# Optimization experiments

Measured on AMD Instinct MI355X. Metric: run time of the kernel, lower is better.

The kernel has to match this reference:

```python
import jax, jax.numpy as jnp
import numpy as np

H = 1024
BATCH, T = 16, 2048

def setup_inputs() -> dict:
    key = jax.random.key(0)
    k1, k2, k3, k4 = jax.random.split(key, 4)
    scale = 1.0 / (H ** 0.5)
    return {
        "u_sequence": jax.random.normal(k1, (BATCH, T, 1), dtype=jnp.float32),
        "A": jax.random.normal(k2, (H, H), dtype=jnp.float32) * scale,
        "B": jax.random.normal(k3, (H, 1), dtype=jnp.float32) * scale,
        "C": jax.random.normal(k4, (1, H), dtype=jnp.float32) * scale,
        "D": jnp.zeros((1,), dtype=jnp.float32),
    }

def reference(u_sequence, A, B, C, D):
    # u_sequence: [Bt, T, 1]
    u = u_sequence[..., 0]            # [Bt, T]
    b_vec = B[:, 0]                   # [H]

    def step(h, u_t):
        # h: [Bt, H], u_t: [Bt]
        h_new = h @ A.T + u_t[:, None] * b_vec[None, :]
        return h_new, h_new

    h0 = jnp.zeros((u.shape[0], H), dtype=u.dtype)
    _, h_stack = jax.lax.scan(step, h0, u.T)   # h_stack: [T, Bt, H]
    h_stack = jnp.swapaxes(h_stack, 0, 1)      # [Bt, T, H]
    y = jnp.einsum("bth,h->bt", h_stack, C[0]) + u * D[0]
    return y[..., None]                         # [Bt, T, 1]
```

## Files before the change

kernel.cpp:

```cpp
#include <hip/hip_runtime.h>

#define HDIM 1024
#define TLEN 2048
#define NBATCH 16

typedef short bf16x8 __attribute__((ext_vector_type(8)));
typedef float floatx4 __attribute__((ext_vector_type(4)));
typedef unsigned short ushort_t;

__device__ __forceinline__ ushort_t f2bf(float x) {
  unsigned u = __float_as_uint(x);
  unsigned r = (u + 0x7FFFu + ((u >> 16) & 1u)) >> 16;
  return (ushort_t)r;
}
__device__ __forceinline__ float bf2f(ushort_t h) {
  return __uint_as_float(((unsigned)h) << 16);
}

#define LSTR 40
#define TSTR 71

__global__ __launch_bounds__(256) void prep(const float* __restrict__ A,
    const float* __restrict__ Bv, const float* __restrict__ Cv,
    ushort_t* __restrict__ Ah, ushort_t* __restrict__ Am, ushort_t* __restrict__ Al,
    ushort_t* __restrict__ ATh, ushort_t* __restrict__ ATm, ushort_t* __restrict__ ATl,
    float* __restrict__ Vc, float* __restrict__ U) {
  __shared__ ushort_t Lt[3 * 64 * TSTR];
  const int tid = threadIdx.x;
  if (blockIdx.x >= 256) {
    int i = (blockIdx.x - 256) * 256 + tid;
    if (i < HDIM) Vc[i] = Bv[i];
    else U[i - HDIM] = Cv[i - HDIM];
    return;
  }
  const int row0 = (blockIdx.x >> 4) * 64, col0 = (blockIdx.x & 15) * 64;
  const int r = tid >> 2, q = tid & 3;
  ushort_t hs[16], ms[16], ls[16];
#pragma unroll
  for (int c4 = 0; c4 < 4; ++c4) {
    float4 a = *(const float4*)&A[(row0 + r) * HDIM + col0 + q * 16 + c4 * 4];
    float av[4] = {a.x, a.y, a.z, a.w};
#pragma unroll
    for (int i = 0; i < 4; ++i) {
      float z = av[i];
      ushort_t h = f2bf(z); float r1 = z - bf2f(h);
      ushort_t mq = f2bf(r1); float r2 = r1 - bf2f(mq);
      ushort_t lq = f2bf(r2);
      hs[c4 * 4 + i] = h; ms[c4 * 4 + i] = mq; ls[c4 * 4 + i] = lq;
    }
  }
  size_t go = (size_t)(row0 + r) * HDIM + col0 + q * 16;
  *(uint4*)&Ah[go] = ((uint4*)hs)[0]; *(uint4*)&Ah[go + 8] = ((uint4*)hs)[1];
  *(uint4*)&Am[go] = ((uint4*)ms)[0]; *(uint4*)&Am[go + 8] = ((uint4*)ms)[1];
  *(uint4*)&Al[go] = ((uint4*)ls)[0]; *(uint4*)&Al[go + 8] = ((uint4*)ls)[1];
#pragma unroll
  for (int i = 0; i < 16; ++i) {
    int c = q * 16 + i;
    Lt[0 * 64 * TSTR + r * TSTR + c] = hs[i];
    Lt[1 * 64 * TSTR + r * TSTR + c] = ms[i];
    Lt[2 * 64 * TSTR + r * TSTR + c] = ls[i];
  }
  __syncthreads();
  const int c = tid >> 2, q2 = tid & 3;
  ushort_t* dsts[3] = {ATh, ATm, ATl};
#pragma unroll
  for (int s = 0; s < 3; ++s) {
    ushort_t tmp[16];
#pragma unroll
    for (int rr = 0; rr < 16; ++rr) tmp[rr] = Lt[s * 64 * TSTR + (q2 * 16 + rr) * TSTR + c];
    size_t gt = (size_t)(col0 + c) * HDIM + row0 + q2 * 16;
    *(uint4*)&dsts[s][gt] = ((uint4*)tmp)[0];
    *(uint4*)&dsts[s][gt + 8] = ((uint4*)tmp)[1];
  }
}

template <int MODE, int NC, bool SIX, bool WRITEL>
__global__ __launch_bounds__(256) void sq_mfma(
    const ushort_t* __restrict__ Xh, const ushort_t* __restrict__ Xm,
    const ushort_t* __restrict__ Xl,
    const ushort_t* __restrict__ XTh, const ushort_t* __restrict__ XTm,
    const ushort_t* __restrict__ XTl,
    ushort_t* __restrict__ Zh, ushort_t* __restrict__ Zm, ushort_t* __restrict__ Zl,
    ushort_t* __restrict__ ZTh, ushort_t* __restrict__ ZTm, ushort_t* __restrict__ ZTl,
    const float* __restrict__ Af, const float* __restrict__ Bvf,
    float* __restrict__ VU) {
  __shared__ ushort_t sm[6 * 64 * LSTR];
  const int tid = threadIdx.x;

  if (blockIdx.x >= 256) {
    const int tb = blockIdx.x - 256;
    const int wv = tb * 4 + (tid >> 6);
    const int lane = tid & 63;
    if (MODE == 0) {
      float acc = 0.f;
      for (int k = lane; k < HDIM; k += 64) acc += Af[(size_t)wv * HDIM + k] * Bvf[k];
      for (int off = 32; off; off >>= 1) acc += __shfl_down(acc, off);
      if (lane == 0) VU[HDIM + wv] = acc;
    } else {
      const ushort_t* Ph = (MODE == 1) ? Xh : XTh;
      const ushort_t* Pm = (MODE == 1) ? Xm : XTm;
      float acc[NC];
#pragma unroll
      for (int n = 0; n < NC; ++n) acc[n] = 0.f;
      for (int k = lane; k < HDIM; k += 64) {
        float a = bf2f(Ph[(size_t)wv * HDIM + k]) + bf2f(Pm[(size_t)wv * HDIM + k]);
#pragma unroll
        for (int n = 0; n < NC; ++n) acc[n] += a * VU[(size_t)n * HDIM + k];
      }
#pragma unroll
      for (int n = 0; n < NC; ++n) {
        float s = acc[n];
        for (int off = 32; off; off >>= 1) s += __shfl_down(s, off);
        if (lane == 0) VU[(size_t)(NC + n) * HDIM + wv] = s;
      }
    }
    return;
  }

  const int bb = blockIdx.x;
  const int xcd = bb & 7, slot = bb >> 3;
  const int tr = 4 * (xcd >> 1) + (slot >> 3);
  const int tc = 8 * (xcd & 1) + (slot & 7);
  const int row0 = tr * 64, col0 = tc * 64;

  const int AH = 0, AM = 64 * LSTR, AL = 2 * 64 * LSTR;
  const int BH = 3 * 64 * LSTR, BM = 4 * 64 * LSTR, BL = 5 * 64 * LSTR;
  const int w = tid >> 6, l = tid & 63, li = l & 15, quad = l >> 4;
  const int sr = tid >> 2, sq4 = tid & 3;

  floatx4 acc0 = {0.f, 0.f, 0.f, 0.f}, acc1 = acc0, acc2 = acc0, acc3 = acc0;

  const int aoff = (w * 16 + li) * LSTR + quad * 8;
  const int b0o = (0 * 16 + li) * LSTR + quad * 8;
  const int b1o = (1 * 16 + li) * LSTR + quad * 8;
  const int b2o = (2 * 16 + li) * LSTR + quad * 8;
  const int b3o = (3 * 16 + li) * LSTR + quad * 8;
  const int soff = sr * LSTR + sq4 * 8;
  const size_t gA = (size_t)(row0 + sr) * HDIM + sq4 * 8;
  const size_t gB = (size_t)(col0 + sr) * HDIM + sq4 * 8;

  uint4 pa0 = *(const uint4*)&Xh[gA], pa1 = *(const uint4*)&Xm[gA];
  uint4 pb0 = *(const uint4*)&XTh[gB], pb1 = *(const uint4*)&XTm[gB];
  uint4 pa2, pb2;
  if (SIX) { pa2 = *(const uint4*)&Xl[gA]; pb2 = *(const uint4*)&XTl[gB]; }

  for (int k0 = 0; k0 < HDIM; k0 += 32) {
    __syncthreads();
    *(uint4*)&sm[AH + soff] = pa0;
    *(uint4*)&sm[AM + soff] = pa1;
    *(uint4*)&sm[BH + soff] = pb0;
    *(uint4*)&sm[BM + soff] = pb1;
    if (SIX) {
      *(uint4*)&sm[AL + soff] = pa2;
      *(uint4*)&sm[BL + soff] = pb2;
    }
    __syncthreads();
    if (k0 + 32 < HDIM) {
      pa0 = *(const uint4*)&Xh[gA + k0 + 32];
      pa1 = *(const uint4*)&Xm[gA + k0 + 32];
      pb0 = *(const uint4*)&XTh[gB + k0 + 32];
      pb1 = *(const uint4*)&XTm[gB + k0 + 32];
      if (SIX) {
        pa2 = *(const uint4*)&Xl[gA + k0 + 32];
        pb2 = *(const uint4*)&XTl[gB + k0 + 32];
      }
    }
    bf16x8 ah = *(const bf16x8*)&sm[AH + aoff];
    bf16x8 am = *(const bf16x8*)&sm[AM + aoff];
    bf16x8 al;
    if (SIX) al = *(const bf16x8*)&sm[AL + aoff];
    {
      bf16x8 bh = *(const bf16x8*)&sm[BH + b0o];
      bf16x8 bm = *(const bf16x8*)&sm[BM + b0o];
      acc0 = __builtin_amdgcn_mfma_f32_16x16x32_bf16(ah, bh, acc0, 0, 0, 0);
      acc0 = __builtin_amdgcn_mfma_f32_16x16x32_bf16(ah, bm, acc0, 0, 0, 0);
      acc0 = __builtin_amdgcn_mfma_f32_16x16x32_bf16(am, bh, acc0, 0, 0, 0);
      acc0 = __builtin_amdgcn_mfma_f32_16x16x32_bf16(am, bm, acc0, 0, 0, 0);
      if (SIX) {
        bf16x8 bl = *(const bf16x8*)&sm[BL + b0o];
        acc0 = __builtin_amdgcn_mfma_f32_16x16x32_bf16(ah, bl, acc0, 0, 0, 0);
        acc0 = __builtin_amdgcn_mfma_f32_16x16x32_bf16(al, bh, acc0, 0, 0, 0);
      }
    }
    {
      bf16x8 bh = *(const bf16x8*)&sm[BH + b1o];
      bf16x8 bm = *(const bf16x8*)&sm[BM + b1o];
      acc1 = __builtin_amdgcn_mfma_f32_16x16x32_bf16(ah, bh, acc1, 0, 0, 0);
      acc1 = __builtin_amdgcn_mfma_f32_16x16x32_bf16(ah, bm, acc1, 0, 0, 0);
      acc1 = __builtin_amdgcn_mfma_f32_16x16x32_bf16(am, bh, acc1, 0, 0, 0);
      acc1 = __builtin_amdgcn_mfma_f32_16x16x32_bf16(am, bm, acc1, 0, 0, 0);
      if (SIX) {
        bf16x8 bl = *(const bf16x8*)&sm[BL + b1o];
        acc1 = __builtin_amdgcn_mfma_f32_16x16x32_bf16(ah, bl, acc1, 0, 0, 0);
        acc1 = __builtin_amdgcn_mfma_f32_16x16x32_bf16(al, bh, acc1, 0, 0, 0);
      }
    }
    {
      bf16x8 bh = *(const bf16x8*)&sm[BH + b2o];
      bf16x8 bm = *(const bf16x8*)&sm[BM + b2o];
      acc2 = __builtin_amdgcn_mfma_f32_16x16x32_bf16(ah, bh, acc2, 0, 0, 0);
      acc2 = __builtin_amdgcn_mfma_f32_16x16x32_bf16(ah, bm, acc2, 0, 0, 0);
      acc2 = __builtin_amdgcn_mfma_f32_16x16x32_bf16(am, bh, acc2, 0, 0, 0);
      acc2 = __builtin_amdgcn_mfma_f32_16x16x32_bf16(am, bm, acc2, 0, 0, 0);
      if (SIX) {
        bf16x8 bl = *(const bf16x8*)&sm[BL + b2o];
        acc2 = __builtin_amdgcn_mfma_f32_16x16x32_bf16(ah, bl, acc2, 0, 0, 0);
        acc2 = __builtin_amdgcn_mfma_f32_16x16x32_bf16(al, bh, acc2, 0, 0, 0);
      }
    }
    {
      bf16x8 bh = *(const bf16x8*)&sm[BH + b3o];
      bf16x8 bm = *(const bf16x8*)&sm[BM + b3o];
      acc3 = __builtin_amdgcn_mfma_f32_16x16x32_bf16(ah, bh, acc3, 0, 0, 0);
      acc3 = __builtin_amdgcn_mfma_f32_16x16x32_bf16(ah, bm, acc3, 0, 0, 0);
      acc3 = __builtin_amdgcn_mfma_f32_16x16x32_bf16(am, bh, acc3, 0, 0, 0);
      acc3 = __builtin_amdgcn_mfma_f32_16x16x32_bf16(am, bm, acc3, 0, 0, 0);
      if (SIX) {
        bf16x8 bl = *(const bf16x8*)&sm[BL + b3o];
        acc3 = __builtin_amdgcn_mfma_f32_16x16x32_bf16(ah, bl, acc3, 0, 0, 0);
        acc3 = __builtin_amdgcn_mfma_f32_16x16x32_bf16(al, bh, acc3, 0, 0, 0);
      }
    }
  }

  __syncthreads();
  floatx4 accs[4] = {acc0, acc1, acc2, acc3};
#pragma unroll
  for (int j = 0; j < 4; ++j) {
#pragma unroll
    for (int e = 0; e < 4; ++e) {
      float z = accs[j][e];
      int rl = w * 16 + quad * 4 + e;
      int cl = j * 16 + li;
      size_t go = (size_t)(row0 + rl) * HDIM + col0 + cl;
      ushort_t h = f2bf(z); float r1 = z - bf2f(h);
      ushort_t mq = f2bf(r1);
      Zh[go] = h; Zm[go] = mq;
      sm[0 * 64 * TSTR + rl * TSTR + cl] = h;
      sm[1 * 64 * TSTR + rl * TSTR + cl] = mq;
      if (WRITEL) {
        ushort_t lq = f2bf(r1 - bf2f(mq));
        Zl[go] = lq;
        sm[2 * 64 * TSTR + rl * TSTR + cl] = lq;
      }
    }
  }
  __syncthreads();
  const int c = tid >> 2, q2 = tid & 3;
  ushort_t* dsts[3] = {ZTh, ZTm, ZTl};
  const int npass = WRITEL ? 3 : 2;
#pragma unroll
  for (int s = 0; s < 3; ++s) {
    if (s >= npass) break;
    ushort_t tmp[16];
#pragma unroll
    for (int rr = 0; rr < 16; ++rr) tmp[rr] = sm[s * 64 * TSTR + (q2 * 16 + rr) * TSTR + c];
    size_t gt = (size_t)(col0 + c) * HDIM + row0 + q2 * 16;
    *(uint4*)&dsts[s][gt] = ((uint4*)tmp)[0];
    *(uint4*)&dsts[s][gt + 8] = ((uint4*)tmp)[1];
  }
}

__global__ __launch_bounds__(256) void utail8(const ushort_t* __restrict__ PTh,
                                              const ushort_t* __restrict__ PTm,
                                              float* __restrict__ U, int dstbase) {
  const int wv = blockIdx.x * 4 + (threadIdx.x >> 6);
  const int lane = threadIdx.x & 63;
  float acc[8];
#pragma unroll
  for (int m = 0; m < 8; ++m) acc[m] = 0.f;
  const float* Usrc = U + (size_t)(dstbase - 8) * HDIM;
  for (int k = lane; k < HDIM; k += 64) {
    float a = bf2f(PTh[(size_t)wv * HDIM + k]) + bf2f(PTm[(size_t)wv * HDIM + k]);
#pragma unroll
    for (int m = 0; m < 8; ++m) acc[m] += a * Usrc[(size_t)m * HDIM + k];
  }
#pragma unroll
  for (int m = 0; m < 8; ++m) {
    float s = acc[m];
    for (int off = 32; off; off >>= 1) s += __shfl_down(s, off);
    if (lane == 0) U[(size_t)(dstbase + m) * HDIM + wv] = s;
  }
}

__global__ __launch_bounds__(256) void wavedotK(const float* __restrict__ U,
                                                const float* __restrict__ Vc,
                                                float* __restrict__ Km) {
  int wv = (blockIdx.x * blockDim.x + threadIdx.x) >> 6;
  int lane = threadIdx.x & 63;
  if (wv >= 32 * 64) return;
  int mr = wv >> 6;
  int nc = wv & 63;
  float s = 0.f;
  for (int k = lane; k < HDIM; k += 64) s += U[mr * HDIM + k] * Vc[nc * HDIM + k];
  for (int off = 32; off; off >>= 1) s += __shfl_down(s, off);
  if (lane == 0) Km[wv] = s;
}

__global__ __launch_bounds__(256) void convk2(const float* __restrict__ u,
                                              const float* __restrict__ Km,
                                              const float* __restrict__ Dv,
                                              float* __restrict__ y) {
  __shared__ float ks[256];
  __shared__ float us[512];
  const int tt = threadIdx.x;
  const int t0 = blockIdx.x * 256;
  const int b = blockIdx.y;
  const float* ub = u + (size_t)b * TLEN;
  const int t = t0 + tt;
  float s = Dv[0] * ub[t];
  for (int mc = 0; mc <= t0; mc += 256) {
    __syncthreads();
    ks[tt] = Km[mc + tt];
    int w0 = t0 - mc - 255;
    int g0 = w0 + tt;
    us[tt] = (g0 >= 0) ? ub[g0] : 0.f;
    int g1 = w0 + 256 + tt;
    us[256 + tt] = (g1 < TLEN) ? ub[g1] : 0.f;
    __syncthreads();
    if (mc < t0) {
#pragma unroll 4
      for (int r = 0; r < 256; r += 4) {
        float4 kv = *(const float4*)&ks[r];
        s += kv.x * us[tt - r + 255];
        s += kv.y * us[tt - r + 254];
        s += kv.z * us[tt - r + 253];
        s += kv.w * us[tt - r + 252];
      }
    } else {
      for (int r = 0; r <= tt; ++r) s += ks[r] * us[tt - r + 255];
    }
  }
  y[(size_t)b * TLEN + t] = s;
}

extern "C" void kernel_launch(void* const* d_in, const int* in_sizes, int n_in,
                              void* d_out, int out_size, void* d_ws, size_t ws_size,
                              hipStream_t stream) {
  const float* u  = (const float*)d_in[0];
  const float* A  = (const float*)d_in[1];
  const float* Bv = (const float*)d_in[2];
  const float* Cv = (const float*)d_in[3];
  const float* Dv = (const float*)d_in[4];
  float* out = (float*)d_out;

  char* wsb = (char*)d_ws;
  size_t off = 0;
  ushort_t* S[2][6];
  for (int s = 0; s < 2; ++s)
    for (int a = 0; a < 6; ++a) { S[s][a] = (ushort_t*)(wsb + off); off += (size_t)2 << 20; }
  float* Vc = (float*)(wsb + off); off += 64 * HDIM * 4;
  float* U  = (float*)(wsb + off); off += 32 * HDIM * 4;
  float* Km = (float*)(wsb + off); off += TLEN * 4;

  const dim3 gsq(512);

#define SQ(MODE, NC, SIX, WRL, IN, OUT, VU)                                    \
  sq_mfma<MODE, NC, SIX, WRL><<<gsq, 256, 0, stream>>>(                        \
      S[IN][0], S[IN][1], S[IN][2], S[IN][3], S[IN][4], S[IN][5],              \
      S[OUT][0], S[OUT][1], S[OUT][2], S[OUT][3], S[OUT][4], S[OUT][5],        \
      A, Bv, VU)

  prep<<<dim3(264), 256, 0, stream>>>(A, Bv, Cv,
      S[0][0], S[0][1], S[0][2], S[0][3], S[0][4], S[0][5], Vc, U);

  SQ(0, 1,  true,  true,  0, 1, Vc);
  SQ(1, 2,  true,  true,  1, 0, Vc);
  SQ(1, 4,  true,  true,  0, 1, Vc);
  SQ(1, 8,  true,  false, 1, 0, Vc);
  SQ(1, 16, false, false, 0, 1, Vc);
  SQ(1, 32, false, false, 1, 0, Vc);
  SQ(2, 1,  false, false, 0, 1, U);
  SQ(2, 2,  false, false, 1, 0, U);
  SQ(2, 4,  false, false, 0, 1, U);
#undef SQ

  utail8<<<dim3(256), 256, 0, stream>>>(S[1][3], S[1][4], U, 8);
  utail8<<<dim3(256), 256, 0, stream>>>(S[1][3], S[1][4], U, 16);
  utail8<<<dim3(256), 256, 0, stream>>>(S[1][3], S[1][4], U, 24);

  wavedotK<<<dim3(512), 256, 0, stream>>>(U, Vc, Km);
  convk2<<<dim3(TLEN / 256, NBATCH), 256, 0, stream>>>(u, Km, Dv, out);
}
```

Baseline: 333.4 us.

## Load MFMA operands directly from global memory with register double-buffering

Replaces the LDS-staged main loop of the split-bf16 squaring GEMM with operand fragments read straight from global memory into registers, using a two-stage ping-pong over 32-wide K chunks. This drops the two barriers per K step and the LDS store/load traffic, and shrinks shared memory to what the epilogue transpose needs. In exchange, each wave redundantly fetches the B fragments for all four column tiles (more global/L2 traffic, since there is no intra-block sharing), and register pressure rises from holding two full sets of operands.

Measured after the change: 576.1 us. 1.73x slower.

```diff
diff --git a/kernel.cpp b/kernel.cpp
--- a/kernel.cpp
+++ b/kernel.cpp
@@ -17,7 +17,6 @@
   return __uint_as_float(((unsigned)h) << 16);
 }
 
-#define LSTR 40
 #define TSTR 71
 
 __global__ __launch_bounds__(256) void prep(const float* __restrict__ A,
@@ -84,7 +83,7 @@
     ushort_t* __restrict__ ZTh, ushort_t* __restrict__ ZTm, ushort_t* __restrict__ ZTl,
     const float* __restrict__ Af, const float* __restrict__ Bvf,
     float* __restrict__ VU) {
-  __shared__ ushort_t sm[6 * 64 * LSTR];
+  __shared__ ushort_t sm[3 * 64 * TSTR];
   const int tid = threadIdx.x;
 
   if (blockIdx.x >= 256) {
@@ -123,108 +122,60 @@
   const int tc = 8 * (xcd & 1) + (slot & 7);
   const int row0 = tr * 64, col0 = tc * 64;
 
-  const int AH = 0, AM = 64 * LSTR, AL = 2 * 64 * LSTR;
-  const int BH = 3 * 64 * LSTR, BM = 4 * 64 * LSTR, BL = 5 * 64 * LSTR;
   const int w = tid >> 6, l = tid & 63, li = l & 15, quad = l >> 4;
-  const int sr = tid >> 2, sq4 = tid & 3;
-
-  floatx4 acc0 = {0.f, 0.f, 0.f, 0.f}, acc1 = acc0, acc2 = acc0, acc3 = acc0;
-
-  const int aoff = (w * 16 + li) * LSTR + quad * 8;
-  const int b0o = (0 * 16 + li) * LSTR + quad * 8;
-  const int b1o = (1 * 16 + li) * LSTR + quad * 8;
-  const int b2o = (2 * 16 + li) * LSTR + quad * 8;
-  const int b3o = (3 * 16 + li) * LSTR + quad * 8;
-  const int soff = sr * LSTR + sq4 * 8;
-  const size_t gA = (size_t)(row0 + sr) * HDIM + sq4 * 8;
-  const size_t gB = (size_t)(col0 + sr) * HDIM + sq4 * 8;
-
-  uint4 pa0 = *(const uint4*)&Xh[gA], pa1 = *(const uint4*)&Xm[gA];
-  uint4 pb0 = *(const uint4*)&XTh[gB], pb1 = *(const uint4*)&XTm[gB];
-  uint4 pa2, pb2;
-  if (SIX) { pa2 = *(const uint4*)&Xl[gA]; pb2 = *(const uint4*)&XTl[gB]; }
-
-  for (int k0 = 0; k0 < HDIM; k0 += 32) {
-    __syncthreads();
-    *(uint4*)&sm[AH + soff] = pa0;
-    *(uint4*)&sm[AM + soff] = pa1;
-    *(uint4*)&sm[BH + soff] = pb0;
-    *(uint4*)&sm[BM + soff] = pb1;
-    if (SIX) {
-      *(uint4*)&sm[AL + soff] = pa2;
-      *(uint4*)&sm[BL + soff] = pb2;
-    }
-    __syncthreads();
-    if (k0 + 32 < HDIM) {
-      pa0 = *(const uint4*)&Xh[gA + k0 + 32];
-      pa1 = *(const uint4*)&Xm[gA + k0 + 32];
-      pb0 = *(const uint4*)&XTh[gB + k0 + 32];
-      pb1 = *(const uint4*)&XTm[gB + k0 + 32];
-      if (SIX) {
-        pa2 = *(const uint4*)&Xl[gA + k0 + 32];
-        pb2 = *(const uint4*)&XTl[gB + k0 + 32];
-      }
-    }
-    bf16x8 ah = *(const bf16x8*)&sm[AH + aoff];
-    bf16x8 am = *(const bf16x8*)&sm[AM + aoff];
-    bf16x8 al;
-    if (SIX) al = *(const bf16x8*)&sm[AL + aoff];
-    {
-      bf16x8 bh = *(const bf16x8*)&sm[BH + b0o];
-      bf16x8 bm = *(const bf16x8*)&sm[BM + b0o];
-      acc0 = __builtin_amdgcn_mfma_f32_16x16x32_bf16(ah, bh, acc0, 0, 0, 0);
-      acc0 = __builtin_amdgcn_mfma_f32_16x16x32_bf16(ah, bm, acc0, 0, 0, 0);
-      acc0 = __builtin_amdgcn_mfma_f32_16x16x32_bf16(am, bh, acc0, 0, 0, 0);
-      acc0 = __builtin_amdgcn_mfma_f32_16x16x32_bf16(am, bm, acc0, 0, 0, 0);
-      if (SIX) {
-        bf16x8 bl = *(const bf16x8*)&sm[BL + b0o];
-        acc0 = __builtin_amdgcn_mfma_f32_16x16x32_bf16(ah, bl, acc0, 0, 0, 0);
-        acc0 = __builtin_amdgcn_mfma_f32_16x16x32_bf16(al, bh, acc0, 0, 0, 0);
-      }
-    }
-    {
-      bf16x8 bh = *(const bf16x8*)&sm[BH + b1o];
-      bf16x8 bm = *(const bf16x8*)&sm[BM + b1o];
-      acc1 = __builtin_amdgcn_mfma_f32_16x16x32_bf16(ah, bh, acc1, 0, 0, 0);
-      acc1 = __builtin_amdgcn_mfma_f32_16x16x32_bf16(ah, bm, acc1, 0, 0, 0);
-      acc1 = __builtin_amdgcn_mfma_f32_16x16x32_bf16(am, bh, acc1, 0, 0, 0);
-      acc1 = __builtin_amdgcn_mfma_f32_16x16x32_bf16(am, bm, acc1, 0, 0, 0);
-      if (SIX) {
-        bf16x8 bl = *(const bf16x8*)&sm[BL + b1o];
-        acc1 = __builtin_amdgcn_mfma_f32_16x16x32_bf16(ah, bl, acc1, 0, 0, 0);
-        acc1 = __builtin_amdgcn_mfma_f32_16x16x32_bf16(al, bh, acc1, 0, 0, 0);
-      }
-    }
-    {
-      bf16x8 bh = *(const bf16x8*)&sm[BH + b2o];
-      bf16x8 bm = *(const bf16x8*)&sm[BM + b2o];
-      acc2 = __builtin_amdgcn_mfma_f32_16x16x32_bf16(ah, bh, acc2, 0, 0, 0);
-      acc2 = __builtin_amdgcn_mfma_f32_16x16x32_bf16(ah, bm, acc2, 0, 0, 0);
-      acc2 = __builtin_amdgcn_mfma_f32_16x16x32_bf16(am, bh, acc2, 0, 0, 0);
-      acc2 = __builtin_amdgcn_mfma_f32_16x16x32_bf16(am, bm, acc2, 0, 0, 0);
-      if (SIX) {
-        bf16x8 bl = *(const bf16x8*)&sm[BL + b2o];
-        acc2 = __builtin_amdgcn_mfma_f32_16x16x32_bf16(ah, bl, acc2, 0, 0, 0);
-        acc2 = __builtin_amdgcn_mfma_f32_16x16x32_bf16(al, bh, acc2, 0, 0, 0);
-      }
-    }
-    {
-      bf16x8 bh = *(const bf16x8*)&sm[BH + b3o];
-      bf16x8 bm = *(const bf16x8*)&sm[BM + b3o];
-      acc3 = __builtin_amdgcn_mfma_f32_16x16x32_bf16(ah, bh, acc3, 0, 0, 0);
-      acc3 = __builtin_amdgcn_mfma_f32_16x16x32_bf16(ah, bm, acc3, 0, 0, 0);
-      acc3 = __builtin_amdgcn_mfma_f32_16x16x32_bf16(am, bh, acc3, 0, 0, 0);
-      acc3 = __builtin_amdgcn_mfma_f32_16x16x32_bf16(am, bm, acc3, 0, 0, 0);
-      if (SIX) {
-        bf16x8 bl = *(const bf16x8*)&sm[BL + b3o];
-        acc3 = __builtin_amdgcn_mfma_f32_16x16x32_bf16(ah, bl, acc3, 0, 0, 0);
-        acc3 = __builtin_amdgcn_mfma_f32_16x16x32_bf16(al, bh, acc3, 0, 0, 0);
-      }
-    }
-  }
-
-  __syncthreads();
-  floatx4 accs[4] = {acc0, acc1, acc2, acc3};
+
+  const size_t aoff = (size_t)(row0 + w * 16 + li) * HDIM + quad * 8;
+  size_t boff[4];
+#pragma unroll
+  for (int j = 0; j < 4; ++j)
+    boff[j] = (size_t)(col0 + j * 16 + li) * HDIM + quad * 8;
+
+  floatx4 accs[4];
+#pragma unroll
+  for (int j = 0; j < 4; ++j) accs[j] = (floatx4){0.f, 0.f, 0.f, 0.f};
+
+  bf16x8 ah0, am0, al0, bh0[4], bm0[4], bl0[4];
+  bf16x8 ah1, am1, al1, bh1[4], bm1[4], bl1[4];
+
+#define LOADF(AH_, AM_, AL_, BH_, BM_, BL_, KOFF)                              \
+  {                                                                            \
+    AH_ = *(const bf16x8*)&Xh[aoff + (KOFF)];                                  \
+    AM_ = *(const bf16x8*)&Xm[aoff + (KOFF)];                                  \
+    if (SIX) AL_ = *(const bf16x8*)&Xl[aoff + (KOFF)];                         \
+    _Pragma("unroll") for (int j = 0; j < 4; ++j) {                            \
+      BH_[j] = *(const bf16x8*)&XTh[boff[j] + (KOFF)];                         \
+      BM_[j] = *(const bf16x8*)&XTm[boff[j] + (KOFF)];                         \
+      if (SIX) BL_[j] = *(const bf16x8*)&XTl[boff[j] + (KOFF)];                \
+    }                                                                          \
+  }
+
+#define DO_TERMS(AH_, AM_, AL_, BH_, BM_, BL_)                                 \
+  {                                                                            \
+    _Pragma("unroll") for (int j = 0; j < 4; ++j) {                            \
+      floatx4 a = accs[j];                                                     \
+      a = __builtin_amdgcn_mfma_f32_16x16x32_bf16(AH_, BH_[j], a, 0, 0, 0);    \
+      a = __builtin_amdgcn_mfma_f32_16x16x32_bf16(AH_, BM_[j], a, 0, 0, 0);    \
+      a = __builtin_amdgcn_mfma_f32_16x16x32_bf16(AM_, BH_[j], a, 0, 0, 0);    \
+      a = __builtin_amdgcn_mfma_f32_16x16x32_bf16(AM_, BM_[j], a, 0, 0, 0);    \
+      if (SIX) {                                                               \
+        a = __builtin_amdgcn_mfma_f32_16x16x32_bf16(AH_, BL_[j], a, 0, 0, 0);  \
+        a = __builtin_amdgcn_mfma_f32_16x16x32_bf16(AL_, BH_[j], a, 0, 0, 0);  \
+      }                                                                        \
+      accs[j] = a;                                                             \
+    }                                                                          \
+  }
+
+  LOADF(ah0, am0, al0, bh0, bm0, bl0, 0);
+  for (int k0 = 0; k0 < HDIM; k0 += 64) {
+    LOADF(ah1, am1, al1, bh1, bm1, bl1, k0 + 32);
+    DO_TERMS(ah0, am0, al0, bh0, bm0, bl0);
+    const int kq = (k0 + 64 < HDIM) ? k0 + 64 : 0;
+    LOADF(ah0, am0, al0, bh0, bm0, bl0, kq);
+    DO_TERMS(ah1, am1, al1, bh1, bm1, bl1);
+  }
+#undef LOADF
+#undef DO_TERMS
+
 #pragma unroll
   for (int j = 0; j < 4; ++j) {
 #pragma unroll
```

## Split-K the repeated-squaring GEMM into two halves with a separate finalize kernel

Applied to the files above, without the earlier changes.

Each 64x64 output tile of the squaring GEMM now gets two blocks, each covering half of K, so 512 GEMM blocks run instead of 256 and more of the GPU's CUs are occupied. The partial sums go to two fp32 scratch matrices. A new finalize kernel adds them and does the bf16 hi/mid/lo split plus the transposed stores that the GEMM epilogue used to do. Shared memory also shrinks when the six-product variant is off. The cost is an extra launch per squaring step and about 8 MB of extra fp32 write and read traffic per step.

Result: no change. 337.7 us (+1.3%).

```diff
diff --git a/kernel.cpp b/kernel.cpp
--- a/kernel.cpp
+++ b/kernel.cpp
@@ -19,6 +19,8 @@
 
 #define LSTR 40
 #define TSTR 71
+
+#define MFMA(A_, B_, C_) __builtin_amdgcn_mfma_f32_16x16x32_bf16(A_, B_, C_, 0, 0, 0)
 
 __global__ __launch_bounds__(256) void prep(const float* __restrict__ A,
     const float* __restrict__ Bv, const float* __restrict__ Cv,
@@ -74,21 +76,22 @@
   }
 }
 
-template <int MODE, int NC, bool SIX, bool WRITEL>
-__global__ __launch_bounds__(256) void sq_mfma(
+template <int MODE, int NC, bool SIX>
+__global__ __launch_bounds__(256) void sq_part(
     const ushort_t* __restrict__ Xh, const ushort_t* __restrict__ Xm,
     const ushort_t* __restrict__ Xl,
     const ushort_t* __restrict__ XTh, const ushort_t* __restrict__ XTm,
     const ushort_t* __restrict__ XTl,
-    ushort_t* __restrict__ Zh, ushort_t* __restrict__ Zm, ushort_t* __restrict__ Zl,
-    ushort_t* __restrict__ ZTh, ushort_t* __restrict__ ZTm, ushort_t* __restrict__ ZTl,
+    float* __restrict__ Zp0, float* __restrict__ Zp1,
     const float* __restrict__ Af, const float* __restrict__ Bvf,
     float* __restrict__ VU) {
-  __shared__ ushort_t sm[6 * 64 * LSTR];
+  constexpr int SLAB = 64 * LSTR;
+  constexpr int NSLAB = SIX ? 6 : 4;
+  __shared__ ushort_t sm[NSLAB * SLAB];
   const int tid = threadIdx.x;
 
-  if (blockIdx.x >= 256) {
-    const int tb = blockIdx.x - 256;
+  if (blockIdx.x >= 512) {
+    const int tb = blockIdx.x - 512;
     const int wv = tb * 4 + (tid >> 6);
     const int lane = tid & 63;
     if (MODE == 0) {
@@ -119,12 +122,15 @@
 
   const int bb = blockIdx.x;
   const int xcd = bb & 7, slot = bb >> 3;
-  const int tr = 4 * (xcd >> 1) + (slot >> 3);
-  const int tc = 8 * (xcd & 1) + (slot & 7);
+  const int kh = slot & 1;
+  const int tr = 4 * (xcd >> 1) + (slot >> 4);
+  const int tc = 8 * (xcd & 1) + ((slot >> 1) & 7);
   const int row0 = tr * 64, col0 = tc * 64;
-
-  const int AH = 0, AM = 64 * LSTR, AL = 2 * 64 * LSTR;
-  const int BH = 3 * 64 * LSTR, BM = 4 * 64 * LSTR, BL = 5 * 64 * LSTR;
+  const int kbase = kh * (HDIM / 2), kend = kbase + HDIM / 2;
+
+  constexpr int AH = 0, AM = SLAB, AL = 2 * SLAB;
+  constexpr int BH = (SIX ? 3 : 2) * SLAB, BM = (SIX ? 4 : 3) * SLAB, BL = 5 * SLAB;
+
   const int w = tid >> 6, l = tid & 63, li = l & 15, quad = l >> 4;
   const int sr = tid >> 2, sq4 = tid & 3;
 
@@ -136,15 +142,15 @@
   const int b2o = (2 * 16 + li) * LSTR + quad * 8;
   const int b3o = (3 * 16 + li) * LSTR + quad * 8;
   const int soff = sr * LSTR + sq4 * 8;
-  const size_t gA = (size_t)(row0 + sr) * HDIM + sq4 * 8;
-  const size_t gB = (size_t)(col0 + sr) * HDIM + sq4 * 8;
+  const size_t gA = (size_t)(row0 + sr) * HDIM + sq4 * 8 + kbase;
+  const size_t gB = (size_t)(col0 + sr) * HDIM + sq4 * 8 + kbase;
 
   uint4 pa0 = *(const uint4*)&Xh[gA], pa1 = *(const uint4*)&Xm[gA];
   uint4 pb0 = *(const uint4*)&XTh[gB], pb1 = *(const uint4*)&XTm[gB];
   uint4 pa2, pb2;
   if (SIX) { pa2 = *(const uint4*)&Xl[gA]; pb2 = *(const uint4*)&XTl[gB]; }
 
-  for (int k0 = 0; k0 < HDIM; k0 += 32) {
+  for (int k0 = kbase; k0 < kend; k0 += 32) {
     __syncthreads();
     *(uint4*)&sm[AH + soff] = pa0;
     *(uint4*)&sm[AM + soff] = pa1;
@@ -155,14 +161,15 @@
       *(uint4*)&sm[BL + soff] = pb2;
     }
     __syncthreads();
-    if (k0 + 32 < HDIM) {
-      pa0 = *(const uint4*)&Xh[gA + k0 + 32];
-      pa1 = *(const uint4*)&Xm[gA + k0 + 32];
-      pb0 = *(const uint4*)&XTh[gB + k0 + 32];
-      pb1 = *(const uint4*)&XTm[gB + k0 + 32];
+    if (k0 + 32 < kend) {
+      const size_t ko = (size_t)(k0 + 32 - kbase);
+      pa0 = *(const uint4*)&Xh[gA + ko];
+      pa1 = *(const uint4*)&Xm[gA + ko];
+      pb0 = *(const uint4*)&XTh[gB + ko];
+      pb1 = *(const uint4*)&XTm[gB + ko];
       if (SIX) {
-        pa2 = *(const uint4*)&Xl[gA + k0 + 32];
-        pb2 = *(const uint4*)&XTl[gB + k0 + 32];
+        pa2 = *(const uint4*)&Xl[gA + ko];
+        pb2 = *(const uint4*)&XTl[gB + ko];
       }
     }
     bf16x8 ah = *(const bf16x8*)&sm[AH + aoff];
@@ -172,78 +179,92 @@
     {
       bf16x8 bh = *(const bf16x8*)&sm[BH + b0o];
       bf16x8 bm = *(const bf16x8*)&sm[BM + b0o];
-      acc0 = __builtin_amdgcn_mfma_f32_16x16x32_bf16(ah, bh, acc0, 0, 0, 0);
-      acc0 = __builtin_amdgcn_mfma_f32_16x16x32_bf16(ah, bm, acc0, 0, 0, 0);
-      acc0 = __builtin_amdgcn_mfma_f32_16x16x32_bf16(am, bh, acc0, 0, 0, 0);
-      acc0 = __builtin_amdgcn_mfma_f32_16x16x32_bf16(am, bm, acc0, 0, 0, 0);
+      acc0 = MFMA(ah, bh, acc0); acc0 = MFMA(ah, bm, acc0);
+      acc0 = MFMA(am, bh, acc0); acc0 = MFMA(am, bm, acc0);
       if (SIX) {
         bf16x8 bl = *(const bf16x8*)&sm[BL + b0o];
-        acc0 = __builtin_amdgcn_mfma_f32_16x16x32_bf16(ah, bl, acc0, 0, 0, 0);
-        acc0 = __builtin_amdgcn_mfma_f32_16x16x32_bf16(al, bh, acc0, 0, 0, 0);
+        acc0 = MFMA(ah, bl, acc0); acc0 = MFMA(al, bh, acc0);
       }
     }
     {
       bf16x8 bh = *(const bf16x8*)&sm[BH + b1o];
       bf16x8 bm = *(const bf16x8*)&sm[BM + b1o];
-      acc1 = __builtin_amdgcn_mfma_f32_16x16x32_bf16(ah, bh, acc1, 0, 0, 0);
-      acc1 = __builtin_amdgcn_mfma_f32_16x16x32_bf16(ah, bm, acc1, 0, 0, 0);
-      acc1 = __builtin_amdgcn_mfma_f32_16x16x32_bf16(am, bh, acc1, 0, 0, 0);
-      acc1 = __builtin_amdgcn_mfma_f32_16x16x32_bf16(am, bm, acc1, 0, 0, 0);
+      acc1 = MFMA(ah, bh, acc1); acc1 = MFMA(ah, bm, acc1);
+      acc1 = MFMA(am, bh, acc1); acc1 = MFMA(am, bm, acc1);
       if (SIX) {
         bf16x8 bl = *(const bf16x8*)&sm[BL + b1o];
-        acc1 = __builtin_amdgcn_mfma_f32_16x16x32_bf16(ah, bl, acc1, 0, 0, 0);
-        acc1 = __builtin_amdgcn_mfma_f32_16x16x32_bf16(al, bh, acc1, 0, 0, 0);
+        acc1 = MFMA(ah, bl, acc1); acc1 = MFMA(al, bh, acc1);
       }
     }
     {
       bf16x8 bh = *(const bf16x8*)&sm[BH + b2o];
       bf16x8 bm = *(const bf16x8*)&sm[BM + b2o];
-      acc2 = __builtin_amdgcn_mfma_f32_16x16x32_bf16(ah, bh, acc2, 0, 0, 0);
-      acc2 = __builtin_amdgcn_mfma_f32_16x16x32_bf16(ah, bm, acc2, 0, 0, 0);
-      acc2 = __builtin_amdgcn_mfma_f32_16x16x32_bf16(am, bh, acc2, 0, 0, 0);
-      acc2 = __builtin_amdgcn_mfma_f32_16x16x32_bf16(am, bm, acc2, 0, 0, 0);
+      acc2 = MFMA(ah, bh, acc2); acc2 = MFMA(ah, bm, acc2);
+      acc2 = MFMA(am, bh, acc2); acc2 = MFMA(am, bm, acc2);
       if (SIX) {
         bf16x8 bl = *(const bf16x8*)&sm[BL + b2o];
-        acc2 = __builtin_amdgcn_mfma_f32_16x16x32_bf16(ah, bl, acc2, 0, 0, 0);
-        acc2 = __builtin_amdgcn_mfma_f32_16x16x32_bf16(al, bh, acc2, 0, 0, 0);
+        acc2 = MFMA(ah, bl, acc2); acc2 = MFMA(al, bh, acc2);
       }
     }
     {
       bf16x8 bh = *(const bf16x8*)&sm[BH + b3o];
       bf16x8 bm = *(const bf16x8*)&sm[BM + b3o];
-      acc3 = __builtin_amdgcn_mfma_f32_16x16x32_bf16(ah, bh, acc3, 0, 0, 0);
-      acc3 = __builtin_amdgcn_mfma_f32_16x16x32_bf16(ah, bm, acc3, 0, 0, 0);
-      acc3 = __builtin_amdgcn_mfma_f32_16x16x32_bf16(am, bh, acc3, 0, 0, 0);
-      acc3 = __builtin_amdgcn_mfma_f32_16x16x32_bf16(am, bm, acc3, 0, 0, 0);
+      acc3 = MFMA(ah, bh, acc3); acc3 = MFMA(ah, bm, acc3);
+      acc3 = MFMA(am, bh, acc3); acc3 = MFMA(am, bm, acc3);
       if (SIX) {
         bf16x8 bl = *(const bf16x8*)&sm[BL + b3o];
-        acc3 = __builtin_amdgcn_mfma_f32_16x16x32_bf16(ah, bl, acc3, 0, 0, 0);
-        acc3 = __builtin_amdgcn_mfma_f32_16x16x32_bf16(al, bh, acc3, 0, 0, 0);
-      }
-    }
-  }
-
-  __syncthreads();
+        acc3 = MFMA(ah, bl, acc3); acc3 = MFMA(al, bh, acc3);
+      }
+    }
+  }
+
+  float* __restrict__ Zp = kh ? Zp1 : Zp0;
   floatx4 accs[4] = {acc0, acc1, acc2, acc3};
 #pragma unroll
-  for (int j = 0; j < 4; ++j) {
+  for (int j = 0; j < 4; ++j)
 #pragma unroll
     for (int e = 0; e < 4; ++e) {
-      float z = accs[j][e];
       int rl = w * 16 + quad * 4 + e;
       int cl = j * 16 + li;
-      size_t go = (size_t)(row0 + rl) * HDIM + col0 + cl;
+      Zp[(size_t)(row0 + rl) * HDIM + col0 + cl] = accs[j][e];
+    }
+}
+
+template <bool WRITEL>
+__global__ __launch_bounds__(256) void finalize(
+    const float* __restrict__ Zp0, const float* __restrict__ Zp1,
+    ushort_t* __restrict__ Zh, ushort_t* __restrict__ Zm, ushort_t* __restrict__ Zl,
+    ushort_t* __restrict__ ZTh, ushort_t* __restrict__ ZTm, ushort_t* __restrict__ ZTl) {
+  __shared__ ushort_t Lt[3 * 64 * TSTR];
+  const int tid = threadIdx.x;
+  const int row0 = (blockIdx.x >> 4) * 64, col0 = (blockIdx.x & 15) * 64;
+  const int r = tid >> 2, q = tid & 3;
+  ushort_t hs[16], ms[16], ls[16];
+#pragma unroll
+  for (int c4 = 0; c4 < 4; ++c4) {
+    size_t gi = (size_t)(row0 + r) * HDIM + col0 + q * 16 + c4 * 4;
+    float4 a = *(const float4*)&Zp0[gi];
+    float4 b = *(const float4*)&Zp1[gi];
+    float av[4] = {a.x + b.x, a.y + b.y, a.z + b.z, a.w + b.w};
+#pragma unroll
+    for (int i = 0; i < 4; ++i) {
+      float z = av[i];
       ushort_t h = f2bf(z); float r1 = z - bf2f(h);
       ushort_t mq = f2bf(r1);
-      Zh[go] = h; Zm[go] = mq;
-      sm[0 * 64 * TSTR + rl * TSTR + cl] = h;
-      sm[1 * 64 * TSTR + rl * TSTR + cl] = mq;
-      if (WRITEL) {
-        ushort_t lq = f2bf(r1 - bf2f(mq));
-        Zl[go] = lq;
-        sm[2 * 64 * TSTR + rl * TSTR + cl] = lq;
-      }
-    }
+      hs[c4 * 4 + i] = h; ms[c4 * 4 + i] = mq;
+      if (WRITEL) ls[c4 * 4 + i] = f2bf(r1 - bf2f(mq));
+    }
+  }
+  size_t go = (size_t)(row0 + r) * HDIM + col0 + q * 16;
+  *(uint4*)&Zh[go] = ((uint4*)hs)[0]; *(uint4*)&Zh[go + 8] = ((uint4*)hs)[1];
+  *(uint4*)&Zm[go] = ((uint4*)ms)[0]; *(uint4*)&Zm[go + 8] = ((uint4*)ms)[1];
+  if (WRITEL) { *(uint4*)&Zl[go] = ((uint4*)ls)[0]; *(uint4*)&Zl[go + 8] = ((uint4*)ls)[1]; }
+#pragma unroll
+  for (int i = 0; i < 16; ++i) {
+    int c = q * 16 + i;
+    Lt[0 * 64 * TSTR + r * TSTR + c] = hs[i];
+    Lt[1 * 64 * TSTR + r * TSTR + c] = ms[i];
+    if (WRITEL) Lt[2 * 64 * TSTR + r * TSTR + c] = ls[i];
   }
   __syncthreads();
   const int c = tid >> 2, q2 = tid & 3;
@@ -254,7 +275,7 @@
     if (s >= npass) break;
     ushort_t tmp[16];
 #pragma unroll
-    for (int rr = 0; rr < 16; ++rr) tmp[rr] = sm[s * 64 * TSTR + (q2 * 16 + rr) * TSTR + c];
+    for (int rr = 0; rr < 16; ++rr) tmp[rr] = Lt[s * 64 * TSTR + (q2 * 16 + rr) * TSTR + c];
     size_t gt = (size_t)(col0 + c) * HDIM + row0 + q2 * 16;
     *(uint4*)&dsts[s][gt] = ((uint4*)tmp)[0];
     *(uint4*)&dsts[s][gt + 8] = ((uint4*)tmp)[1];
@@ -349,17 +370,21 @@
   ushort_t* S[2][6];
   for (int s = 0; s < 2; ++s)
     for (int a = 0; a < 6; ++a) { S[s][a] = (ushort_t*)(wsb + off); off += (size_t)2 << 20; }
+  float* Zp0 = (float*)(wsb + off); off += (size_t)HDIM * HDIM * 4;
+  float* Zp1 = (float*)(wsb + off); off += (size_t)HDIM * HDIM * 4;
   float* Vc = (float*)(wsb + off); off += 64 * HDIM * 4;
   float* U  = (float*)(wsb + off); off += 32 * HDIM * 4;
   float* Km = (float*)(wsb + off); off += TLEN * 4;
 
-  const dim3 gsq(512);
+  const dim3 gsq(768);
 
 #define SQ(MODE, NC, SIX, WRL, IN, OUT, VU)                                    \
-  sq_mfma<MODE, NC, SIX, WRL><<<gsq, 256, 0, stream>>>(                        \
+  sq_part<MODE, NC, SIX><<<gsq, 256, 0, stream>>>(                             \
       S[IN][0], S[IN][1], S[IN][2], S[IN][3], S[IN][4], S[IN][5],              \
-      S[OUT][0], S[OUT][1], S[OUT][2], S[OUT][3], S[OUT][4], S[OUT][5],        \
-      A, Bv, VU)
+      Zp0, Zp1, A, Bv, VU);                                                    \
+  finalize<WRL><<<dim3(256), 256, 0, stream>>>(                                \
+      Zp0, Zp1,                                                                \
+      S[OUT][0], S[OUT][1], S[OUT][2], S[OUT][3], S[OUT][4], S[OUT][5])
 
   prep<<<dim3(264), 256, 0, stream>>>(A, Bv, Cv,
       S[0][0], S[0][1], S[0][2], S[0][3], S[0][4], S[0][5], Vc, U);
```
